# Kernel optimization log

Measured on AMD Instinct MI355X. Metric: run time of the kernel, lower is better.

The kernel has to match this reference:

```python
import jax, jax.numpy as jnp
import numpy as np

B, S, K = 64, 512, 16
USERS, ITEMS = 100000, 100000
DU, DI = 64, 192
H = DU + DI  # 256, hidden_dim = user_dim + item_dim


def _layernorm(x, g, b):
    m = jnp.mean(x, -1, keepdims=True)
    v = jnp.var(x, -1, keepdims=True)
    return (x - m) / jnp.sqrt(v + 1e-5) * g + b


def setup_inputs() -> dict:
    key = jax.random.key(0)
    ks = jax.random.split(key, 40)
    g = lambda i, shape, s=0.02: jax.random.normal(ks[i], shape, jnp.float32) * s
    return dict(
        users=jax.random.randint(ks[0], (B,), 0, USERS),
        candidates=jax.random.randint(ks[1], (B, S), 0, ITEMS),
        targets_idx=jax.random.randint(ks[2], (B, K), 0, S),
        embed_user=g(3, (USERS, DU), 1.0),
        embed_item=g(4, (ITEMS, DI), 1.0),
        Wq=g(5, (H, H)), bq=jnp.zeros((H,), jnp.float32),
        Wk=g(6, (H, H)), bk=jnp.zeros((H,), jnp.float32),
        Wv=g(7, (H, H)), bv=jnp.zeros((H,), jnp.float32),
        Wo=g(8, (H, H)), bo=jnp.zeros((H,), jnp.float32),
        ln1_g=jnp.ones((H,), jnp.float32), ln1_b=jnp.zeros((H,), jnp.float32),
        Wf1=g(9, (H, 4 * H)), bf1=jnp.zeros((4 * H,), jnp.float32),
        Wf2=g(10, (4 * H, H)), bf2=jnp.zeros((H,), jnp.float32),
        ln2_g=jnp.ones((H,), jnp.float32), ln2_b=jnp.zeros((H,), jnp.float32),
        W_ih=g(11, (4 * H, H)), W_hh=g(12, (4 * H, H)),
        b_ih=jnp.zeros((4 * H,), jnp.float32), b_hh=jnp.zeros((4 * H,), jnp.float32),
        W_D1=g(13, (2 * H, H)), W_D2=g(14, (H, H)),
        bias1=jnp.zeros((H,), jnp.float32), V_D1=g(15, (H,)),
        W_D3=g(16, (3 * H, H)), W_D4=g(17, (H, H)),
        bias2=jnp.zeros((H,), jnp.float32), V_D2=g(18, (H,)),
    )


def reference(users, candidates, targets_idx, embed_user, embed_item,
              Wq, bq, Wk, bk, Wv, bv, Wo, bo, ln1_g, ln1_b,
              Wf1, bf1, Wf2, bf2, ln2_g, ln2_b,
              W_ih, W_hh, b_ih, b_hh,
              W_D1, W_D2, bias1, V_D1, W_D3, W_D4, bias2, V_D2):
    Bc, Sc = candidates.shape
    # encode: item||user embeddings -> 1-layer, 1-head transformer encoder
    ue = jnp.broadcast_to(embed_user[users][:, None, :], (Bc, Sc, DU))
    x = jnp.concatenate([embed_item[candidates], ue], -1)  # (B,S,H)
    q = x @ Wq + bq
    kk = x @ Wk + bk
    v = x @ Wv + bv
    att = jax.nn.softmax(jnp.einsum('bqh,bkh->bqk', q, kk) / jnp.sqrt(jnp.float32(H)), -1)
    x = _layernorm(x + jnp.einsum('bqk,bkh->bqh', att, v) @ Wo + bo, ln1_g, ln1_b)
    x = _layernorm(x + jax.nn.relu(x @ Wf1 + bf1) @ Wf2 + bf2, ln2_g, ln2_b)
    enc = x                                           # (B,S,H) candidates_embed
    enc_t = jnp.transpose(enc, (1, 0, 2))             # (S,B,H)
    # gather target embeddings; step 0 input is zeros (targets_embed[0] unused)
    tgt = jnp.take_along_axis(enc, targets_idx[..., None], axis=1)  # (B,K,H)
    inputs = jnp.transpose(tgt, (1, 0, 2)).at[0].set(0.0)           # (K,B,H)

    def cell(hc, xin):  # custom LSTMCell with packed (h,c) state of size 2H
        h, c = jnp.split(hc, 2, -1)
        gates = xin @ W_ih.T + b_ih + h @ W_hh.T + b_hh
        i_, f_, g_, o_ = jnp.split(gates, 4, -1)
        c = jax.nn.sigmoid(f_) * c + jax.nn.sigmoid(i_) * jnp.tanh(g_)
        h = jax.nn.sigmoid(o_) * jnp.tanh(c)
        hc = jnp.concatenate([h, c], -1)
        return hc, hc

    hc0 = jnp.zeros((Bc, 2 * H), x.dtype)
    _, dec = jax.lax.scan(cell, hc0, inputs)          # (K,B,2H)
    # glimpse attention (Bahdanau additive, softmax over enc axis=1)
    e = jnp.tanh((dec @ W_D1)[:, None] + (enc_t @ W_D2)[None] + bias1)  # (K,S,B,H)
    a = jax.nn.softmax(e @ V_D1, axis=1)              # (K,S,B)
    glim = jnp.einsum('ksb,sbh->kbh', a, enc_t)       # (K,B,H)
    gcat = jnp.concatenate([dec, glim], -1)           # (K,B,3H)
    # pointer attention -> raw logits (output_prob=False, no masks)
    e2 = jnp.tanh((gcat @ W_D3)[:, None] + (enc_t @ W_D4)[None] + bias2)  # (K,S,B,H)
    logits = e2 @ V_D2                                # (K,S,B)
    return jnp.transpose(logits, (2, 0, 1))           # (B,K,S)
```

## Files before the change

kernel.cpp:

```cpp
#include <hip/hip_runtime.h>
#include <hip/hip_bf16.h>
#include <math.h>

#define B_   64
#define S_   512
#define K_   16
#define H_   256
#define H4_  1024

typedef __attribute__((ext_vector_type(4))) float f32x4;
typedef __attribute__((ext_vector_type(8))) short bf16x8;

__device__ __forceinline__ float wave_reduce_sum(float v) {
#pragma unroll
  for (int off = 32; off; off >>= 1) v += __shfl_down(v, off, 64);
  return v;
}
__device__ __forceinline__ float wave_reduce_max(float v) {
#pragma unroll
  for (int off = 32; off; off >>= 1) v = fmaxf(v, __shfl_down(v, off, 64));
  return v;
}
__device__ __forceinline__ float tanh_fast(float x) {
  const float e = __expf(2.f * x);
  return 1.f - __fdividef(2.f, e + 1.f);
}
__device__ __forceinline__ float sigmoid_fast(float x) {
  return __fdividef(1.f, 1.f + __expf(-x));
}
__device__ __forceinline__ ushort f2bf(float f) {
  union { float f; unsigned u; } v; v.f = f;
  unsigned r = v.u + 0x7FFFu + ((v.u >> 16) & 1u);
  return (ushort)(r >> 16);
}

__global__ void gather_x(const int* __restrict__ users, const int* __restrict__ cand,
                         const float* __restrict__ eu, const float* __restrict__ ei,
                         float* __restrict__ x, ushort* __restrict__ xb)
{
  int idx = blockIdx.x * 256 + threadIdx.x;
  int h  = idx & (H_ - 1);
  int bs = idx >> 8;
  int b  = bs >> 9;
  float v;
  if (h < 192) v = ei[(long)cand[bs] * 192 + h];
  else         v = eu[(long)users[b] * 64 + (h - 192)];
  x[idx] = v;
  xb[idx] = f2bf(v);
}

__global__ __launch_bounds__(256) void tcvt(const float* __restrict__ in, ushort* __restrict__ out,
                                            int R, int C)
{
  __shared__ float t[32][33];
  const int c0 = blockIdx.x * 32, r0 = blockIdx.y * 32;
  const int tx = threadIdx.x & 31, ty = threadIdx.x >> 5;
#pragma unroll
  for (int i = 0; i < 4; ++i)
    t[ty + 8 * i][tx] = in[(long)(r0 + ty + 8 * i) * C + c0 + tx];
  __syncthreads();
#pragma unroll
  for (int i = 0; i < 4; ++i)
    out[(long)(c0 + ty + 8 * i) * R + r0 + tx] = f2bf(t[tx][ty + 8 * i]);
}

__global__ __launch_bounds__(256) void tcvt6(
    const float* __restrict__ i0, ushort* __restrict__ o0,
    const float* __restrict__ i1, ushort* __restrict__ o1,
    const float* __restrict__ i2, ushort* __restrict__ o2,
    const float* __restrict__ i3, ushort* __restrict__ o3,
    const float* __restrict__ i4, ushort* __restrict__ o4,
    const float* __restrict__ i5, ushort* __restrict__ o5)
{
  __shared__ float t[32][33];
  const float* in; ushort* out;
  switch (blockIdx.z) {
    case 0: in = i0; out = o0; break;
    case 1: in = i1; out = o1; break;
    case 2: in = i2; out = o2; break;
    case 3: in = i3; out = o3; break;
    case 4: in = i4; out = o4; break;
    default: in = i5; out = o5; break;
  }
  const int c0 = blockIdx.x * 32, r0 = blockIdx.y * 32;
  const int tx = threadIdx.x & 31, ty = threadIdx.x >> 5;
#pragma unroll
  for (int i = 0; i < 4; ++i)
    t[ty + 8 * i][tx] = in[(long)(r0 + ty + 8 * i) * 256 + c0 + tx];
  __syncthreads();
#pragma unroll
  for (int i = 0; i < 4; ++i)
    out[(long)(c0 + ty + 8 * i) * 256 + r0 + tx] = f2bf(t[tx][ty + 8 * i]);
}

__global__ void cvtflat(const float* __restrict__ in, ushort* __restrict__ out)
{
  int idx = blockIdx.x * 256 + threadIdx.x;
  out[idx] = f2bf(in[idx]);
}

template<int OM, bool RELU>
__global__ __launch_bounds__(256) void gemm_bf16(
    const ushort* __restrict__ A, const ushort* __restrict__ BT,
    const float* __restrict__ bias, void* __restrict__ Cv,
    int K, int ldA, int ldB, int ldC, long sA, long sB, long sC)
{
  __shared__ ushort Al[128][40];
  __shared__ ushort Bl[128][40];
  const int bx = blockIdx.x, by = blockIdx.y, bz = blockIdx.z;
  A  += (long)bz * sA + (long)by * 128 * ldA;
  BT += (long)bz * sB + (long)bx * 128 * ldB;
  const int tid = threadIdx.x, lane = tid & 63, wave = tid >> 6;
  const int wr = wave >> 1, wc = wave & 1;
  const int fr = lane & 15, fq = lane >> 4;
  const int srow = tid & 127;
  const int scol = (tid >> 7) * 16;

  const f32x4 fzero = {0.f, 0.f, 0.f, 0.f};
  f32x4 acc[4][4];
#pragma unroll
  for (int i = 0; i < 4; ++i)
#pragma unroll
    for (int j = 0; j < 4; ++j) acc[i][j] = fzero;

  for (int k0 = 0; k0 < K; k0 += 32) {
    const ushort* ap = A  + (long)srow * ldA + k0 + scol;
    const ushort* bp = BT + (long)srow * ldB + k0 + scol;
    *(uint4*)&Al[srow][scol]     = *(const uint4*)(ap);
    *(uint4*)&Al[srow][scol + 8] = *(const uint4*)(ap + 8);
    *(uint4*)&Bl[srow][scol]     = *(const uint4*)(bp);
    *(uint4*)&Bl[srow][scol + 8] = *(const uint4*)(bp + 8);
    __syncthreads();
    bf16x8 af[4], bfr[4];
#pragma unroll
    for (int i = 0; i < 4; ++i) af[i]  = *(const bf16x8*)&Al[wr * 64 + i * 16 + fr][fq * 8];
#pragma unroll
    for (int j = 0; j < 4; ++j) bfr[j] = *(const bf16x8*)&Bl[wc * 64 + j * 16 + fr][fq * 8];
#pragma unroll
    for (int i = 0; i < 4; ++i)
#pragma unroll
      for (int j = 0; j < 4; ++j)
        acc[i][j] = __builtin_amdgcn_mfma_f32_16x16x32_bf16(af[i], bfr[j], acc[i][j], 0, 0, 0);
    __syncthreads();
  }

  const int rowb = by * 128 + wr * 64 + fq * 4;
  const int colb = bx * 128 + wc * 64 + fr;
#pragma unroll
  for (int j = 0; j < 4; ++j) {
    const int colg = colb + j * 16;
    const float bb = bias ? bias[colg] : 0.f;
#pragma unroll
    for (int i = 0; i < 4; ++i) {
      const int rowg = rowb + i * 16;
      if (OM == 0) {
        float* C = (float*)Cv;
#pragma unroll
        for (int r = 0; r < 4; ++r) {
          float o = acc[i][j][r] + bb;
          if (RELU) o = fmaxf(o, 0.f);
          C[(long)bz * sC + (long)(rowg + r) * ldC + colg] = o;
        }
      } else if (OM == 1) {
        ushort* C = (ushort*)Cv;
#pragma unroll
        for (int r = 0; r < 4; ++r) {
          float o = acc[i][j][r] + bb;
          if (RELU) o = fmaxf(o, 0.f);
          C[(long)bz * sC + (long)(rowg + r) * ldC + colg] = f2bf(o);
        }
      } else if (OM == 2) {
        float* C = (float*)Cv;
        const long ct = ((long)(rowg >> 9) * H_ + colg) * S_ + (rowg & 511);
        float4 o;
        o.x = acc[i][j][0] + bb; o.y = acc[i][j][1] + bb;
        o.z = acc[i][j][2] + bb; o.w = acc[i][j][3] + bb;
        *(float4*)&C[ct] = o;
      } else {
        ushort* C = (ushort*)Cv;
        const long ct = ((long)(rowg >> 9) * H_ + colg) * S_ + (rowg & 511);
        ushort4 o;
        o.x = f2bf(acc[i][j][0] + bb); o.y = f2bf(acc[i][j][1] + bb);
        o.z = f2bf(acc[i][j][2] + bb); o.w = f2bf(acc[i][j][3] + bb);
        *(ushort4*)&C[ct] = o;
      }
    }
  }
}

__global__ __launch_bounds__(256) void attn_softmax(const float* __restrict__ att,
                                                    ushort* __restrict__ attb)
{
  __shared__ float red[4];
  const long row = blockIdx.x;
  const float* p = att + row * S_;
  const int t = threadIdx.x, lane = t & 63, wid = t >> 6;
  float v0 = p[t] * 0.0625f, v1 = p[t + 256] * 0.0625f;
  float m = wave_reduce_max(fmaxf(v0, v1));
  if (!lane) red[wid] = m;
  __syncthreads();
  const float bm = fmaxf(fmaxf(red[0], red[1]), fmaxf(red[2], red[3]));
  const float e0 = __expf(v0 - bm), e1 = __expf(v1 - bm);
  float s = wave_reduce_sum(e0 + e1);
  __syncthreads();
  if (!lane) red[wid] = s;
  __syncthreads();
  const float inv = __fdividef(1.f, red[0] + red[1] + red[2] + red[3]);
  ushort* q = attb + row * S_;
  q[t] = f2bf(e0 * inv); q[t + 256] = f2bf(e1 * inv);
}

__global__ __launch_bounds__(256) void ln_res(float* __restrict__ x, const float* __restrict__ y,
                                              const float* __restrict__ g, const float* __restrict__ b,
                                              ushort* __restrict__ xb)
{
  __shared__ float red[4];
  const long row = blockIdx.x;
  const int t = threadIdx.x, lane = t & 63, wid = t >> 6;
  float v = x[row * H_ + t] + y[row * H_ + t];
  float s = wave_reduce_sum(v);
  if (!lane) red[wid] = s;
  __syncthreads();
  const float mean = (red[0] + red[1] + red[2] + red[3]) * (1.f / H_);
  const float d = v - mean;
  float s2 = wave_reduce_sum(d * d);
  __syncthreads();
  if (!lane) red[wid] = s2;
  __syncthreads();
  const float var = (red[0] + red[1] + red[2] + red[3]) * (1.f / H_);
  const float o = d * rsqrtf(var + 1e-5f) * g[t] + b[t];
  x[row * H_ + t] = o;
  xb[row * H_ + t] = f2bf(o);
}

__global__ void gather_inputs(const int* __restrict__ tidx, const ushort* __restrict__ encb,
                              ushort* __restrict__ inpb)
{
  int idx = blockIdx.x * 256 + threadIdx.x;
  int h = idx & 255, kb = idx >> 8;
  int b = kb & 63, k = kb >> 6;
  ushort v = 0;
  if (k > 0) {
    int s = tidx[b * K_ + k];
    v = encb[((long)b * S_ + s) * H_ + h];
  }
  inpb[idx] = v;
}

__global__ __launch_bounds__(256) void lstm_mfma(const float* __restrict__ Xp,
                                                 const ushort* __restrict__ Whhb,
                                                 const float* __restrict__ b_hh,
                                                 float* __restrict__ dec)
{
  __shared__ ushort hsb[H_];
  __shared__ float gates[H4_];
  const int b = blockIdx.x, tid = threadIdx.x;
  const int lane = tid & 63, wave = tid >> 6;
  const int fr = lane & 15, fq = lane >> 4;
  const int n0 = wave * 256;
  if (tid < 128) ((uint*)hsb)[tid] = 0;
  float c = 0.f;
  const int j = tid;
  const float bh0 = b_hh[j], bh1 = b_hh[256 + j], bh2 = b_hh[512 + j], bh3 = b_hh[768 + j];
  __syncthreads();
  for (int step = 0; step < K_; ++step) {
    bf16x8 af[8];
#pragma unroll
    for (int kc = 0; kc < 8; ++kc)
      af[kc] = *(const bf16x8*)&hsb[kc * 32 + fq * 8];
#pragma unroll 4
    for (int nt = 0; nt < 16; ++nt) {
      const ushort* wp = Whhb + (long)(n0 + nt * 16 + fr) * 256 + fq * 8;
      f32x4 acc = {0.f, 0.f, 0.f, 0.f};
#pragma unroll
      for (int kc = 0; kc < 8; ++kc) {
        const bf16x8 bf = *(const bf16x8*)(wp + kc * 32);
        acc = __builtin_amdgcn_mfma_f32_16x16x32_bf16(af[kc], bf, acc, 0, 0, 0);
      }
      if (lane < 16) gates[n0 + nt * 16 + lane] = acc[0];
    }
    __syncthreads();
    {
      const long xrow = ((long)step * B_ + b) * H4_ + j;
      const float gi = gates[j]       + Xp[xrow]       + bh0;
      const float gf = gates[256 + j] + Xp[xrow + 256] + bh1;
      const float gg = gates[512 + j] + Xp[xrow + 512] + bh2;
      const float go = gates[768 + j] + Xp[xrow + 768] + bh3;
      c = sigmoid_fast(gf) * c + sigmoid_fast(gi) * tanh_fast(gg);
      const float h = sigmoid_fast(go) * tanh_fast(c);
      const long rw = ((long)step * B_ + b) * (2 * H_);
      dec[rw + j] = h;
      dec[rw + H_ + j] = c;
      hsb[j] = f2bf(h);
    }
    __syncthreads();
  }
}

__global__ __launch_bounds__(256) void glimpse_kernel(
    const float* __restrict__ decW1, const float* __restrict__ encW2T,
    const float* __restrict__ enc, const float* __restrict__ bias1,
    const float* __restrict__ V1, float* __restrict__ glim)
{
  __shared__ float dv[H_], vd[H_], sc[S_], red[4];
  const int bid = blockIdx.x;
  const int b = bid & 63;
  const int t = threadIdx.x, lane = t & 63, wv = t >> 6;
  dv[t] = decW1[(long)bid * H_ + t] + bias1[t];
  vd[t] = V1[t];
  __syncthreads();
  const float* ebase = encW2T + (long)b * H_ * S_;
  float a0 = 0.f, a1 = 0.f;
#pragma unroll 4
  for (int h = 0; h < H_; ++h) {
    const float d = dv[h], w = vd[h];
    const float* r = ebase + (long)h * S_;
    a0 += tanh_fast(d + r[t]) * w;
    a1 += tanh_fast(d + r[t + 256]) * w;
  }
  float m = wave_reduce_max(fmaxf(a0, a1));
  if (!lane) red[wv] = m;
  __syncthreads();
  const float bm = fmaxf(fmaxf(red[0], red[1]), fmaxf(red[2], red[3]));
  const float e0 = __expf(a0 - bm), e1 = __expf(a1 - bm);
  float ssum = wave_reduce_sum(e0 + e1);
  __syncthreads();
  if (!lane) red[wv] = ssum;
  __syncthreads();
  const float inv = __fdividef(1.f, red[0] + red[1] + red[2] + red[3]);
  sc[t] = e0 * inv; sc[t + 256] = e1 * inv;
  __syncthreads();
  float acc = 0.f;
  const float* eb = enc + (long)b * S_ * H_ + t;
#pragma unroll 4
  for (int s = 0; s < S_; ++s) acc += sc[s] * eb[(long)s * H_];
  glim[(long)bid * H_ + t] = acc;
}

__global__ void concat_gcat(const float* __restrict__ dec, const float* __restrict__ glim,
                            ushort* __restrict__ gcatb)
{
  int idx = blockIdx.x * 256 + threadIdx.x;
  int j = idx % 768, row = idx / 768;
  float v = (j < 512) ? dec[(long)row * 512 + j] : glim[(long)row * 256 + (j - 512)];
  gcatb[idx] = f2bf(v);
}

__global__ __launch_bounds__(256) void pointer_kernel(
    const float* __restrict__ gW3, const float* __restrict__ encW4T,
    const float* __restrict__ bias2, const float* __restrict__ V2,
    float* __restrict__ out)
{
  __shared__ float dv[H_], vd[H_];
  const int bid = blockIdx.x;
  const int b = bid & 63, k = bid >> 6;
  const int t = threadIdx.x;
  dv[t] = gW3[(long)bid * H_ + t] + bias2[t];
  vd[t] = V2[t];
  __syncthreads();
  const float* ebase = encW4T + (long)b * H_ * S_;
  float a0 = 0.f, a1 = 0.f;
#pragma unroll 4
  for (int h = 0; h < H_; ++h) {
    const float d = dv[h], w = vd[h];
    const float* r = ebase + (long)h * S_;
    a0 += tanh_fast(d + r[t]) * w;
    a1 += tanh_fast(d + r[t + 256]) * w;
  }
  const long ro = ((long)b * K_ + k) * S_;
  out[ro + t] = a0;
  out[ro + 256 + t] = a1;
}

extern "C" void kernel_launch(void* const* d_in, const int* in_sizes, int n_in,
                              void* d_out, int out_size, void* d_ws, size_t ws_size,
                              hipStream_t stream)
{
  const int*   users = (const int*)d_in[0];
  const int*   cand  = (const int*)d_in[1];
  const int*   tidx  = (const int*)d_in[2];
  const float* eu    = (const float*)d_in[3];
  const float* ei    = (const float*)d_in[4];
  const float* Wq    = (const float*)d_in[5];
  const float* bq    = (const float*)d_in[6];
  const float* Wk    = (const float*)d_in[7];
  const float* bk    = (const float*)d_in[8];
  const float* Wv    = (const float*)d_in[9];
  const float* bv    = (const float*)d_in[10];
  const float* Wo    = (const float*)d_in[11];
  const float* bo    = (const float*)d_in[12];
  const float* ln1g  = (const float*)d_in[13];
  const float* ln1b  = (const float*)d_in[14];
  const float* Wf1   = (const float*)d_in[15];
  const float* bf1   = (const float*)d_in[16];
  const float* Wf2   = (const float*)d_in[17];
  const float* bf2   = (const float*)d_in[18];
  const float* ln2g  = (const float*)d_in[19];
  const float* ln2b  = (const float*)d_in[20];
  const float* W_ih  = (const float*)d_in[21];
  const float* W_hh  = (const float*)d_in[22];
  const float* b_ih  = (const float*)d_in[23];
  const float* b_hh  = (const float*)d_in[24];
  const float* W_D1  = (const float*)d_in[25];
  const float* W_D2  = (const float*)d_in[26];
  const float* bias1 = (const float*)d_in[27];
  const float* V_D1  = (const float*)d_in[28];
  const float* W_D3  = (const float*)d_in[29];
  const float* W_D4  = (const float*)d_in[30];
  const float* bias2 = (const float*)d_in[31];
  const float* V_D2  = (const float*)d_in[32];

  float* ws = (float*)d_ws;
  float*  x      = ws;
  ushort* xb     = (ushort*)(ws + 8388608);
  ushort* qb     = (ushort*)(ws + 12582912);
  ushort* kb     = (ushort*)(ws + 16777216);
  ushort* vTb    = (ushort*)(ws + 20971520);
  ushort* aob    = (ushort*)(ws + 25165824);
  ushort* attb   = (ushort*)(ws + 29360128);
  float*  ych    = ws + 31457280;
  ushort* wts    = (ushort*)(ws + 33554432);
  float*  att    = ws + 34603008;
  ushort* midb   = (ushort*)att;
  float*  sm     = ws + 38797312;
  float*  encW2T = ws + 12582912;
  float*  encW4T = ws + 20971520;

  ushort* WqT  = wts;
  ushort* WkT  = WqT  + 65536;
  ushort* WvT  = WkT  + 65536;
  ushort* WoT  = WvT  + 65536;
  ushort* Wf1T = WoT  + 65536;
  ushort* Wf2T = Wf1T + 262144;
  ushort* WD1T = Wf2T + 262144;
  ushort* WD2T = WD1T + 131072;
  ushort* WD3T = WD2T + 65536;
  ushort* WD4T = WD3T + 196608;
  ushort* Wihb = WD4T + 65536;

  ushort* inpb   = (ushort*)sm;
  float*  Xp     = sm + 131072;
  ushort* Whhb   = (ushort*)(sm + 1179648);
  float*  dec    = sm + 1441792;
  ushort* decb   = (ushort*)(sm + 1966080);
  float*  decW1  = sm + 2228224;
  float*  glim   = sm + 2490368;
  ushort* gcatb  = (ushort*)(sm + 2752512);
  float*  gcatW3 = sm + 3145728;

  float* out = (float*)d_out;
  const long SH = (long)S_ * H_;

  tcvt6<<<dim3(8,8,6), dim3(256), 0, stream>>>(Wq, WqT, Wk, WkT, Wv, WvT,
                                               Wo, WoT, W_D2, WD2T, W_D4, WD4T);
  tcvt<<<dim3(32,8),  dim3(256), 0, stream>>>(Wf1,  Wf1T, 256, 1024);
  tcvt<<<dim3(8,32),  dim3(256), 0, stream>>>(Wf2,  Wf2T, 1024, 256);
  tcvt<<<dim3(8,16),  dim3(256), 0, stream>>>(W_D1, WD1T, 512, 256);
  tcvt<<<dim3(8,24),  dim3(256), 0, stream>>>(W_D3, WD3T, 768, 256);
  cvtflat<<<dim3(1024), dim3(256), 0, stream>>>(W_ih, Wihb);
  cvtflat<<<dim3(1024), dim3(256), 0, stream>>>(W_hh, Whhb);

  gather_x<<<dim3(32768), dim3(256), 0, stream>>>(users, cand, eu, ei, x, xb);

  gemm_bf16<1,false><<<dim3(2,256), dim3(256), 0, stream>>>(xb, WqT, bq, qb,  256, 256, 256, 256, 0,0,0);
  gemm_bf16<1,false><<<dim3(2,256), dim3(256), 0, stream>>>(xb, WkT, bk, kb,  256, 256, 256, 256, 0,0,0);
  gemm_bf16<3,false><<<dim3(2,256), dim3(256), 0, stream>>>(xb, WvT, bv, vTb, 256, 256, 256, 0,   0,0,0);

  for (int c = 0; c < 4; ++c) {
    const long qo = (long)c * 16 * SH;
    gemm_bf16<0,false><<<dim3(4,4,16), dim3(256), 0, stream>>>(
        qb + qo, kb + qo, nullptr, att, 256, 256, 256, 512, SH, SH, (long)S_*S_);
    attn_softmax<<<dim3(16*S_), dim3(256), 0, stream>>>(att, attb);
    gemm_bf16<1,false><<<dim3(2,4,16), dim3(256), 0, stream>>>(
        attb, vTb + qo, nullptr, aob + qo, 512, 512, 512, 256, (long)S_*S_, SH, SH);
  }

  for (int c = 0; c < 4; ++c) {
    const long off = (long)c * 8192 * H_;
    gemm_bf16<0,false><<<dim3(2,64), dim3(256), 0, stream>>>(aob + off, WoT, bo, ych, 256, 256, 256, 256, 0,0,0);
    ln_res<<<dim3(8192), dim3(256), 0, stream>>>(x + off, ych, ln1g, ln1b, xb + off);
  }

  for (int c = 0; c < 4; ++c) {
    const long off = (long)c * 8192 * H_;
    gemm_bf16<1,true ><<<dim3(8,64), dim3(256), 0, stream>>>(xb + off, Wf1T, bf1, midb, 256, 256, 256, 1024, 0,0,0);
    gemm_bf16<0,false><<<dim3(2,64), dim3(256), 0, stream>>>(midb, Wf2T, bf2, ych, 1024, 1024, 1024, 256, 0,0,0);
    ln_res<<<dim3(8192), dim3(256), 0, stream>>>(x + off, ych, ln2g, ln2b, xb + off);
  }

  gemm_bf16<2,false><<<dim3(2,256), dim3(256), 0, stream>>>(xb, WD2T, nullptr, encW2T, 256, 256, 256, 0, 0,0,0);
  gemm_bf16<2,false><<<dim3(2,256), dim3(256), 0, stream>>>(xb, WD4T, nullptr, encW4T, 256, 256, 256, 0, 0,0,0);

  gather_inputs<<<dim3(1024), dim3(256), 0, stream>>>(tidx, xb, inpb);
  gemm_bf16<0,false><<<dim3(8,8), dim3(256), 0, stream>>>(inpb, Wihb, b_ih, Xp, 256, 256, 256, 1024, 0,0,0);
  lstm_mfma<<<dim3(B_), dim3(256), 0, stream>>>(Xp, Whhb, b_hh, dec);

  cvtflat<<<dim3(2048), dim3(256), 0, stream>>>(dec, decb);
  gemm_bf16<0,false><<<dim3(2,8), dim3(256), 0, stream>>>(decb, WD1T, nullptr, decW1, 512, 512, 512, 256, 0,0,0);
  glimpse_kernel<<<dim3(K_*B_), dim3(256), 0, stream>>>(decW1, encW2T, x, bias1, V_D1, glim);

  concat_gcat<<<dim3(3072), dim3(256), 0, stream>>>(dec, glim, gcatb);
  gemm_bf16<0,false><<<dim3(2,8), dim3(256), 0, stream>>>(gcatb, WD3T, nullptr, gcatW3, 768, 768, 768, 256, 0,0,0);
  pointer_kernel<<<dim3(K_*B_), dim3(256), 0, stream>>>(gcatW3, encW4T, bias2, V_D2, out);
}
```

Baseline: 1.267 ms.

## Pre-swizzle W_hh into MFMA fragment layout and double LSTM block waves

Adds a prep kernel that reorders W_hh into the per-lane bf16x8 fragment order used by the MFMA, so each wave's weight loads become contiguous, coalesced 16-byte reads. The LSTM kernel now runs 512 threads (8 waves), each handling 8 gate tiles instead of 16, which halves the serial MFMA chain per wave in every recurrent step. Only the first 256 threads do the elementwise cell update. The cost is idle threads during that update and a slightly different prep kernel.

```diff
diff --git a/kernel.cpp b/kernel.cpp
--- a/kernel.cpp
+++ b/kernel.cpp
@@ -97,6 +97,18 @@
 {
   int idx = blockIdx.x * 256 + threadIdx.x;
   out[idx] = f2bf(in[idx]);
+}
+
+__global__ void whh_prep(const float* __restrict__ W, ushort* __restrict__ Wp)
+{
+  int idx = blockIdx.x * 256 + threadIdx.x;
+  const int i    = idx & 7;
+  const int lane = (idx >> 3) & 63;
+  const int kc   = (idx >> 9) & 7;
+  const int ntg  = idx >> 12;
+  const int n = ntg * 16 + (lane & 15);
+  const int k = kc * 32 + (lane >> 4) * 8 + i;
+  Wp[idx] = f2bf(W[n * 256 + k]);
 }
 
 template<int OM, bool RELU>
@@ -247,8 +259,8 @@
   inpb[idx] = v;
 }
 
-__global__ __launch_bounds__(256) void lstm_mfma(const float* __restrict__ Xp,
-                                                 const ushort* __restrict__ Whhb,
+__global__ __launch_bounds__(512) void lstm_mfma(const float* __restrict__ Xp,
+                                                 const ushort* __restrict__ Wp,
                                                  const float* __restrict__ b_hh,
                                                  float* __restrict__ dec)
 {
@@ -256,31 +268,34 @@
   __shared__ float gates[H4_];
   const int b = blockIdx.x, tid = threadIdx.x;
   const int lane = tid & 63, wave = tid >> 6;
-  const int fr = lane & 15, fq = lane >> 4;
-  const int n0 = wave * 256;
+  const int fq = lane >> 4;
   if (tid < 128) ((uint*)hsb)[tid] = 0;
   float c = 0.f;
-  const int j = tid;
-  const float bh0 = b_hh[j], bh1 = b_hh[256 + j], bh2 = b_hh[512 + j], bh3 = b_hh[768 + j];
+  float bh0 = 0.f, bh1 = 0.f, bh2 = 0.f, bh3 = 0.f;
+  if (tid < 256) {
+    bh0 = b_hh[tid]; bh1 = b_hh[256 + tid]; bh2 = b_hh[512 + tid]; bh3 = b_hh[768 + tid];
+  }
   __syncthreads();
   for (int step = 0; step < K_; ++step) {
     bf16x8 af[8];
 #pragma unroll
     for (int kc = 0; kc < 8; ++kc)
       af[kc] = *(const bf16x8*)&hsb[kc * 32 + fq * 8];
-#pragma unroll 4
-    for (int nt = 0; nt < 16; ++nt) {
-      const ushort* wp = Whhb + (long)(n0 + nt * 16 + fr) * 256 + fq * 8;
+#pragma unroll 2
+    for (int nt = 0; nt < 8; ++nt) {
+      const int ntg = wave * 8 + nt;
+      const ushort* wp = Wp + ((long)(ntg * 8) * 64 + lane) * 8;
       f32x4 acc = {0.f, 0.f, 0.f, 0.f};
 #pragma unroll
       for (int kc = 0; kc < 8; ++kc) {
-        const bf16x8 bf = *(const bf16x8*)(wp + kc * 32);
+        const bf16x8 bf = *(const bf16x8*)(wp + kc * 512);
         acc = __builtin_amdgcn_mfma_f32_16x16x32_bf16(af[kc], bf, acc, 0, 0, 0);
       }
-      if (lane < 16) gates[n0 + nt * 16 + lane] = acc[0];
+      if (lane < 16) gates[ntg * 16 + lane] = acc[0];
     }
     __syncthreads();
-    {
+    if (tid < 256) {
+      const int j = tid;
       const long xrow = ((long)step * B_ + b) * H4_ + j;
       const float gi = gates[j]       + Xp[xrow]       + bh0;
       const float gf = gates[256 + j] + Xp[xrow + 256] + bh1;
@@ -440,7 +455,7 @@
 
   ushort* inpb   = (ushort*)sm;
   float*  Xp     = sm + 131072;
-  ushort* Whhb   = (ushort*)(sm + 1179648);
+  ushort* Wp     = (ushort*)(sm + 1179648);
   float*  dec    = sm + 1441792;
   ushort* decb   = (ushort*)(sm + 1966080);
   float*  decW1  = sm + 2228224;
@@ -458,7 +473,7 @@
   tcvt<<<dim3(8,16),  dim3(256), 0, stream>>>(W_D1, WD1T, 512, 256);
   tcvt<<<dim3(8,24),  dim3(256), 0, stream>>>(W_D3, WD3T, 768, 256);
   cvtflat<<<dim3(1024), dim3(256), 0, stream>>>(W_ih, Wihb);
-  cvtflat<<<dim3(1024), dim3(256), 0, stream>>>(W_hh, Whhb);
+  whh_prep<<<dim3(1024), dim3(256), 0, stream>>>(W_hh, Wp);
 
   gather_x<<<dim3(32768), dim3(256), 0, stream>>>(users, cand, eu, ei, x, xb);
 
@@ -493,7 +508,7 @@
 
   gather_inputs<<<dim3(1024), dim3(256), 0, stream>>>(tidx, xb, inpb);
   gemm_bf16<0,false><<<dim3(8,8), dim3(256), 0, stream>>>(inpb, Wihb, b_ih, Xp, 256, 256, 256, 1024, 0,0,0);
-  lstm_mfma<<<dim3(B_), dim3(256), 0, stream>>>(Xp, Whhb, b_hh, dec);
+  lstm_mfma<<<dim3(B_), dim3(512), 0, stream>>>(Xp, Wp, b_hh, dec);
 
   cvtflat<<<dim3(2048), dim3(256), 0, stream>>>(dec, decb);
   gemm_bf16<0,false><<<dim3(2,8), dim3(256), 0, stream>>>(decb, WD1T, nullptr, decW1, 512, 512, 512, 256, 0,0,0);
```

New measurement: 1.103 ms. -12.9%, faster.
